# Kernel optimization log

Hardware: AMD Instinct MI355X
Metric: run time of the kernel (lower is better)

## Reference

```python
import jax, jax.numpy as jnp
import numpy as np

B = 4096          # graphs (frames)
NPG = 22          # players per frame
N = B * NPG       # total nodes
E = B * NPG * (NPG - 1)
D_BB = 256        # backbone_dout == GRNN hidden
D_NODE = 128      # raw node feature dim
D_PROJ = 256      # cfg.proj_dout
D_GIN = 64        # glob_din
D_GOUT = 128      # cfg.glob_dout
D_IN = D_BB + D_PROJ  # GRNN input dim = 512


def setup_inputs() -> dict:
    key = jax.random.key(0)
    ks = jax.random.split(key, 24)
    def w(k, shape):
        return jax.random.normal(k, shape, jnp.float32) * 0.05
    inp = {
        "z": jax.random.normal(ks[0], (N, D_BB), jnp.float32),
        "u": jax.random.normal(ks[1], (B, D_GIN), jnp.float32),
        "x": jax.random.normal(ks[2], (N, D_NODE), jnp.float32),
        # edge_index is unused math-wise because GConvGRU is built with K=1 ChebConvs
        "edge_index": jax.random.randint(ks[3], (2, E), 0, N, dtype=jnp.int32),
        "batch": jnp.repeat(jnp.arange(B, dtype=jnp.int32), NPG),
        "batch_size": B,
        "prev_h": jax.random.normal(ks[4], (N, D_BB), jnp.float32),
        # fusion params
        "w_proj": w(ks[5], (D_NODE, D_PROJ)), "b_proj": jnp.zeros((D_PROJ,), jnp.float32),
        "w_glob": w(ks[6], (D_GIN, D_GOUT)), "b_glob": jnp.zeros((D_GOUT,), jnp.float32),
        # GConvGRU (K=1 ChebConv == linear) gate params: update z, reset r, candidate h
        "W_xz": w(ks[7], (D_IN, D_BB)),  "b_xz": jnp.zeros((D_BB,), jnp.float32),
        "W_hz": w(ks[8], (D_BB, D_BB)),  "b_hz": jnp.zeros((D_BB,), jnp.float32),
        "W_xr": w(ks[9], (D_IN, D_BB)),  "b_xr": jnp.zeros((D_BB,), jnp.float32),
        "W_hr": w(ks[10], (D_BB, D_BB)), "b_hr": jnp.zeros((D_BB,), jnp.float32),
        "W_xh": w(ks[11], (D_IN, D_BB)), "b_xh": jnp.zeros((D_BB,), jnp.float32),
        "W_hh": w(ks[12], (D_BB, D_BB)), "b_hh": jnp.zeros((D_BB,), jnp.float32),
    }
    return inp


def reference(z, u, x, edge_index, batch, batch_size, prev_h,
              w_proj, b_proj, w_glob, b_glob,
              W_xz, b_xz, W_hz, b_hz,
              W_xr, b_xr, W_hr, b_hr,
              W_xh, b_xh, W_hh, b_hh):
    # --- GraphGlobalFusion: mean readout + relu(Linear(u)) + concat ---
    sums = jax.ops.segment_sum(z, batch, num_segments=batch_size)            # [B, D_BB]
    cnts = jax.ops.segment_sum(jnp.ones((z.shape[0], 1), z.dtype), batch,
                               num_segments=batch_size)                      # [B, 1]
    graph_emb = sums / jnp.maximum(cnts, 1.0)
    glob_emb = jax.nn.relu(u @ w_glob + b_glob)                              # [B, D_GOUT]
    fused = jnp.concatenate([graph_emb, glob_emb], axis=-1)                  # [B, D_BB+D_GOUT]

    # --- node mode: raw feature projection, then GConvGRU (K=1 -> linear gates) ---
    x_proj = jax.nn.relu(x @ w_proj + b_proj)                                # [N, D_PROJ]
    xin = jnp.concatenate([z, x_proj], axis=-1)                              # [N, D_IN]
    Z = jax.nn.sigmoid(xin @ W_xz + b_xz + prev_h @ W_hz + b_hz)
    R = jax.nn.sigmoid(xin @ W_xr + b_xr + prev_h @ W_hr + b_hr)
    H_tilde = jnp.tanh(xin @ W_xh + b_xh + (prev_h * R) @ W_hh + b_hh)
    h = Z * prev_h + (1.0 - Z) * H_tilde                                     # [N, D_BB]
    return (fused, h)
```

## Files before the change

### kernel.cpp

```cpp
#include <hip/hip_runtime.h>
#include <hip/hip_bf16.h>

#define NNODES 90112
#define BGRAPH 4096
#define NPG 22
#define DBB 256
#define DNODE 128
#define DPROJ 256
#define DGIN 64
#define DGOUT 128

#define WTG_OFF   32768
#define WTHH_OFF  622592
#define WS_BF16_ELEMS 688128

typedef __attribute__((ext_vector_type(8))) short bf16x8;
typedef __attribute__((ext_vector_type(4))) short bf16x4;
typedef __attribute__((ext_vector_type(4))) float f32x4;

__device__ __forceinline__ short f2bf(float f) {
  __hip_bfloat16 h = __float2bfloat16(f);
  return *reinterpret_cast<short*>(&h);
}
__device__ __forceinline__ float bf2f(short s) {
  union { unsigned int u; float f; } c;
  c.u = ((unsigned int)(unsigned short)s) << 16;
  return c.f;
}
__device__ __forceinline__ float fsig(float xv) {
  return __fdividef(1.0f, 1.0f + __expf(-xv));
}
__device__ __forceinline__ float ftanh(float xv) {
  return 1.0f - __fdividef(2.0f, __expf(2.0f * xv) + 1.0f);
}

#define DMA16(gsrc, ldst)                                                        \
  __builtin_amdgcn_global_load_lds(                                              \
      (const __attribute__((address_space(1))) void*)(gsrc),                     \
      (__attribute__((address_space(3))) void*)(ldst), 16, 0, 0)

#define VMWAIT(N) do { asm volatile("s_waitcnt vmcnt(" #N ")" ::: "memory");     \
                       __builtin_amdgcn_sched_barrier(0); } while (0)
#define LBAR() do { asm volatile("s_waitcnt lgkmcnt(0)" ::: "memory");           \
                    __builtin_amdgcn_s_barrier(); } while (0)

__global__ void pack_weights(const float* __restrict__ w_proj,
                             const float* __restrict__ W_xz, const float* __restrict__ W_hz,
                             const float* __restrict__ W_xr, const float* __restrict__ W_hr,
                             const float* __restrict__ W_xh, const float* __restrict__ W_hh,
                             const float* __restrict__ b_xz, const float* __restrict__ b_hz,
                             const float* __restrict__ b_xr, const float* __restrict__ b_hr,
                             const float* __restrict__ b_xh, const float* __restrict__ b_hh,
                             __hip_bfloat16* __restrict__ wsb, float* __restrict__ wsf) {
  int i = blockIdx.x * 256 + threadIdx.x;
  if (i < 32768) {
    int c = i >> 7, k = i & 127;
    wsb[i] = __float2bfloat16(w_proj[k * DPROJ + c]);
  } else if (i < WTHH_OFF) {
    int j = i - WTG_OFF;
    int kc  = j / 24576;
    int rem = j - kc * 24576;
    int ct  = rem >> 9;
    int q   = rem & 511;
    int l   = q >> 3, e = q & 7;
    int l15 = l & 15, kg = l >> 4;
    int k   = kc * 32 + kg * 8 + e;
    int g   = ct >> 4;
    int c   = (ct & 15) * 16 + l15;
    float v;
    if (g == 0)      v = (k < 512) ? W_xz[k * 256 + c] : W_hz[(k - 512) * 256 + c];
    else if (g == 1) v = (k < 512) ? W_xr[k * 256 + c] : W_hr[(k - 512) * 256 + c];
    else             v = (k < 512) ? W_xh[k * 256 + c] : 0.0f;
    wsb[i] = __float2bfloat16(v);
  } else if (i < WS_BF16_ELEMS) {
    int j = i - WTHH_OFF;
    int kc  = j >> 13;
    int rem = j & 8191;
    int ct  = rem >> 9;
    int q   = rem & 511;
    int l   = q >> 3, e = q & 7;
    int l15 = l & 15, kg = l >> 4;
    int k   = kc * 32 + kg * 8 + e;
    int c   = ct * 16 + l15;
    wsb[i] = __float2bfloat16(W_hh[k * 256 + c]);
  }
  if (i < 256) {
    wsf[i]       = b_xz[i] + b_hz[i];
    wsf[256 + i] = b_xr[i] + b_hr[i];
    wsf[512 + i] = b_xh[i] + b_hh[i];
  }
}

__global__ void fused_head(const float* __restrict__ z, const float* __restrict__ u,
                           const float* __restrict__ w_glob, const float* __restrict__ b_glob,
                           float* __restrict__ out) {
  int b = blockIdx.x;
  int t = threadIdx.x;
  __shared__ float us[DGIN];
  if (t < DGIN) us[t] = u[b * DGIN + t];
  __syncthreads();
  const float* zb = z + (size_t)b * NPG * DBB;
  #pragma unroll
  for (int half = 0; half < 2; ++half) {
    int c = t + half * 128;
    float s = 0.f;
    #pragma unroll
    for (int r = 0; r < NPG; ++r) s += zb[r * DBB + c];
    out[(size_t)b * 384 + c] = s * (1.0f / NPG);
  }
  float acc = b_glob[t];
  #pragma unroll
  for (int k = 0; k < DGIN; ++k) acc += us[k] * w_glob[k * DGOUT + t];
  out[(size_t)b * 384 + 256 + t] = fmaxf(acc, 0.f);
}

#define MFMA16(a, b, c) __builtin_amdgcn_mfma_f32_16x16x32_bf16(a, b, c, 0, 0, 0)

__global__ __launch_bounds__(1024)
void grnn_main(const float* __restrict__ z, const float* __restrict__ x,
               const float* __restrict__ prev_h, const float* __restrict__ b_proj,
               const __hip_bfloat16* __restrict__ wsb, const float* __restrict__ wsf,
               float* __restrict__ h_out) {
  __shared__ __align__(16) __hip_bfloat16 Wb[2][24576];
  __shared__ __align__(16) __hip_bfloat16 ActC[2][64 * 40];
  __shared__ __align__(16) __hip_bfloat16 XP[64 * 256];

  const int r0   = blockIdx.x * 64;
  const int tid  = threadIdx.x;
  const int wid  = tid >> 6;
  const int lane = tid & 63;
  const int l15  = lane & 15;
  const int lg   = lane >> 4;
  const int c0   = wid * 16;
  const int cgrp = (c0 >> 3) + (lg >> 1);
  const int lgl  = (lg & 1) * 4;

  const __hip_bfloat16* wpk = wsb + WTG_OFF;
  const __hip_bfloat16* hpk = wsb + WTHH_OFF;

  {
    int row = tid >> 4, c8 = tid & 15;
    const float* p = x + (size_t)(r0 + row) * DNODE + c8 * 8;
    f32x4 f0 = *(const f32x4*)p;
    f32x4 f1 = *(const f32x4*)(p + 4);
    bf16x8 o;
    o[0]=f2bf(f0[0]); o[1]=f2bf(f0[1]); o[2]=f2bf(f0[2]); o[3]=f2bf(f0[3]);
    o[4]=f2bf(f1[0]); o[5]=f2bf(f1[1]); o[6]=f2bf(f1[2]); o[7]=f2bf(f1[3]);
    *(bf16x8*)&Wb[1][row * 128 + (c8 ^ (row & 7)) * 8] = o;
  }
  __syncthreads();

  #pragma unroll
  for (int gs = 0; gs < 3; ++gs) {
    int ct = gs * 16 + wid;
    DMA16(wpk + ((size_t)(0 * 48 + ct) * 64 + lane) * 8, &Wb[0][ct * 512]);
  }
  f32x4 accp[4] = {};
  {
    const __hip_bfloat16* wp0 = wsb + (size_t)(c0 + l15) * DNODE + lg * 8;
    #pragma unroll
    for (int kb = 0; kb < 4; ++kb) {
      bf16x8 wp = *(const bf16x8*)(wp0 + kb * 32);
      const int gk = kb * 4 + lg;
      bf16x8 act[4];
      #pragma unroll
      for (int rt = 0; rt < 4; ++rt) {
        const int row = rt * 16 + l15;
        act[rt] = *(const bf16x8*)&Wb[1][row * 128 + (gk ^ (row & 7)) * 8];
      }
      __builtin_amdgcn_s_setprio(1);
      #pragma unroll
      for (int rt = 0; rt < 4; ++rt)
        accp[rt] = MFMA16(wp, act[rt], accp[rt]);
      __builtin_amdgcn_s_setprio(0);
    }
  }
  {
    float4 bp4 = *(const float4*)&b_proj[c0 + lg * 4];
    #pragma unroll
    for (int rt = 0; rt < 4; ++rt) {
      int r = rt * 16 + l15;
      bf16x4 o;
      o[0] = f2bf(fmaxf(accp[rt][0] + bp4.x, 0.f));
      o[1] = f2bf(fmaxf(accp[rt][1] + bp4.y, 0.f));
      o[2] = f2bf(fmaxf(accp[rt][2] + bp4.z, 0.f));
      o[3] = f2bf(fmaxf(accp[rt][3] + bp4.w, 0.f));
      *(bf16x4*)&XP[r * 256 + ((cgrp ^ (r & 7)) * 8) + lgl] = o;
    }
  }
  {
    int row = tid >> 4, c2 = (tid & 15) * 2;
    const float* p = z + (size_t)(r0 + row) * DBB + c2;
    float a = p[0], b = p[1];
    unsigned int pk = (unsigned int)(unsigned short)f2bf(a) |
                      ((unsigned int)(unsigned short)f2bf(b) << 16);
    *(unsigned int*)&ActC[0][row * 40 + (c2 >> 3) * 8 + (c2 & 7)] = pk;
  }
  __syncthreads();

  f32x4 accz[4] = {}, accr[4] = {}, acch[4] = {};
  #pragma unroll
  for (int kc = 0; kc < 24; ++kc) {
    const int kn = kc + 1;
    if (kn < 8 || (kn >= 16 && kn < 24)) {
      const float* src = (kn < 8) ? z : prev_h;
      const int kofs = (kn < 8 ? kn : kn - 16) * 32;
      int row = tid >> 4, c2 = (tid & 15) * 2;
      const float* p = src + (size_t)(r0 + row) * DBB + kofs + c2;
      float a = p[0], b = p[1];
      unsigned int pk = (unsigned int)(unsigned short)f2bf(a) |
                        ((unsigned int)(unsigned short)f2bf(b) << 16);
      *(unsigned int*)&ActC[kn & 1][row * 40 + (c2 >> 3) * 8 + (c2 & 7)] = pk;
    }
    __builtin_amdgcn_sched_barrier(0);
    if (kn < 24) {
      const int ns = (kn < 16) ? 3 : 2;
      #pragma unroll
      for (int gs = 0; gs < 3; ++gs) {
        if (gs < ns) {
          int ct = gs * 16 + wid;
          DMA16(wpk + ((size_t)(kn * 48 + ct) * 64 + lane) * 8, &Wb[kn & 1][ct * 512]);
        }
      }
    }
    __builtin_amdgcn_sched_barrier(0);
    if (kc < 8 || kc >= 16) LBAR();
    if (kc < 15)      VMWAIT(3);
    else if (kc < 23) VMWAIT(2);
    else              VMWAIT(0);
    bf16x8 act[4];
    #pragma unroll
    for (int rt = 0; rt < 4; ++rt) {
      const int row = rt * 16 + l15;
      if (kc < 8 || kc >= 16)
        act[rt] = *(const bf16x8*)&ActC[kc & 1][row * 40 + lg * 8];
      else {
        const int gk = (kc - 8) * 4 + lg;
        act[rt] = *(const bf16x8*)&XP[row * 256 + (gk ^ (row & 7)) * 8];
      }
    }
    bf16x8 wz = *(const bf16x8*)&Wb[kc & 1][(0 * 16 + wid) * 512 + lane * 8];
    bf16x8 wr = *(const bf16x8*)&Wb[kc & 1][(1 * 16 + wid) * 512 + lane * 8];
    bf16x8 wh;
    if (kc < 16) wh = *(const bf16x8*)&Wb[kc & 1][(2 * 16 + wid) * 512 + lane * 8];
    __builtin_amdgcn_s_setprio(1);
    #pragma unroll
    for (int rt = 0; rt < 4; ++rt) {
      accz[rt] = MFMA16(wz, act[rt], accz[rt]);
      accr[rt] = MFMA16(wr, act[rt], accr[rt]);
      if (kc < 16) acch[rt] = MFMA16(wh, act[rt], acch[rt]);
    }
    __builtin_amdgcn_s_setprio(0);
    if (kc < 7 || (kc >= 16 && kc < 23)) LBAR();
  }

  DMA16(hpk + ((size_t)(0 * 16 + wid) * 64 + lane) * 8, &Wb[0][wid * 512]);
  f32x4 phv[4];
  {
    float4 br4 = *(const float4*)&wsf[256 + c0 + lg * 4];
    #pragma unroll
    for (int rt = 0; rt < 4; ++rt) {
      int r = rt * 16 + l15;
      phv[rt] = *(const f32x4*)&prev_h[(size_t)(r0 + r) * DBB + c0 + lg * 4];
      bf16x4 o;
      o[0] = f2bf(phv[rt][0] * fsig(accr[rt][0] + br4.x));
      o[1] = f2bf(phv[rt][1] * fsig(accr[rt][1] + br4.y));
      o[2] = f2bf(phv[rt][2] * fsig(accr[rt][2] + br4.z));
      o[3] = f2bf(phv[rt][3] * fsig(accr[rt][3] + br4.w));
      *(bf16x4*)&XP[r * 256 + ((cgrp ^ (r & 7)) * 8) + lgl] = o;
    }
  }
  LBAR();

  #pragma unroll
  for (int s = 0; s < 8; ++s) {
    if (s < 7)
      DMA16(hpk + ((size_t)((s + 1) * 16 + wid) * 64 + lane) * 8, &Wb[(s + 1) & 1][wid * 512]);
    __builtin_amdgcn_sched_barrier(0);
    if (s < 7) VMWAIT(1); else VMWAIT(0);
    bf16x8 act[4];
    #pragma unroll
    for (int rt = 0; rt < 4; ++rt) {
      const int row = rt * 16 + l15;
      const int gk = s * 4 + lg;
      act[rt] = *(const bf16x8*)&XP[row * 256 + (gk ^ (row & 7)) * 8];
    }
    bf16x8 wv = *(const bf16x8*)&Wb[s & 1][wid * 512 + lane * 8];
    __builtin_amdgcn_s_setprio(1);
    #pragma unroll
    for (int rt = 0; rt < 4; ++rt)
      acch[rt] = MFMA16(wv, act[rt], acch[rt]);
    __builtin_amdgcn_s_setprio(0);
  }

  {
    float4 bz4 = *(const float4*)&wsf[c0 + lg * 4];
    float4 bh4 = *(const float4*)&wsf[512 + c0 + lg * 4];
    #pragma unroll
    for (int rt = 0; rt < 4; ++rt) {
      int r = rt * 16 + l15;
      f32x4 hv;
      float zg = fsig(accz[rt][0] + bz4.x);
      hv[0] = zg * phv[rt][0] + (1.f - zg) * ftanh(acch[rt][0] + bh4.x);
      zg = fsig(accz[rt][1] + bz4.y);
      hv[1] = zg * phv[rt][1] + (1.f - zg) * ftanh(acch[rt][1] + bh4.y);
      zg = fsig(accz[rt][2] + bz4.z);
      hv[2] = zg * phv[rt][2] + (1.f - zg) * ftanh(acch[rt][2] + bh4.z);
      zg = fsig(accz[rt][3] + bz4.w);
      hv[3] = zg * phv[rt][3] + (1.f - zg) * ftanh(acch[rt][3] + bh4.w);
      *(f32x4*)&h_out[(size_t)(r0 + r) * DBB + c0 + lg * 4] = hv;
    }
  }
}

extern "C" void kernel_launch(void* const* d_in, const int* in_sizes, int n_in,
                              void* d_out, int out_size, void* d_ws, size_t ws_size,
                              hipStream_t stream) {
  const float* z      = (const float*)d_in[0];
  const float* u      = (const float*)d_in[1];
  const float* x      = (const float*)d_in[2];
  const float* prev_h = (const float*)d_in[6];
  const float* w_proj = (const float*)d_in[7];
  const float* b_proj = (const float*)d_in[8];
  const float* w_glob = (const float*)d_in[9];
  const float* b_glob = (const float*)d_in[10];
  const float* W_xz   = (const float*)d_in[11];
  const float* b_xz   = (const float*)d_in[12];
  const float* W_hz   = (const float*)d_in[13];
  const float* b_hz   = (const float*)d_in[14];
  const float* W_xr   = (const float*)d_in[15];
  const float* b_xr   = (const float*)d_in[16];
  const float* W_hr   = (const float*)d_in[17];
  const float* b_hr   = (const float*)d_in[18];
  const float* W_xh   = (const float*)d_in[19];
  const float* b_xh   = (const float*)d_in[20];
  const float* W_hh   = (const float*)d_in[21];
  const float* b_hh   = (const float*)d_in[22];

  __hip_bfloat16* wsb = (__hip_bfloat16*)d_ws;
  float* wsf = (float*)((char*)d_ws + (size_t)WS_BF16_ELEMS * 2);

  float* fused = (float*)d_out;
  float* h_out = fused + (size_t)BGRAPH * 384;

  pack_weights<<<dim3(WS_BF16_ELEMS / 256), dim3(256), 0, stream>>>(
      w_proj, W_xz, W_hz, W_xr, W_hr, W_xh, W_hh,
      b_xz, b_hz, b_xr, b_hr, b_xh, b_hh, wsb, wsf);

  fused_head<<<dim3(BGRAPH), dim3(128), 0, stream>>>(z, u, w_glob, b_glob, fused);

  grnn_main<<<dim3(NNODES / 64), dim3(1024), 0, stream>>>(
      z, x, prev_h, b_proj, wsb, wsf, h_out);
}
```

Baseline: 234.8 us.

## Deepen weight DMA pipeline to two stages ahead with per-gate waits

```diff
diff --git a/kernel.cpp b/kernel.cpp
--- a/kernel.cpp
+++ b/kernel.cpp
@@ -17,6 +17,7 @@
 typedef __attribute__((ext_vector_type(8))) short bf16x8;
 typedef __attribute__((ext_vector_type(4))) short bf16x4;
 typedef __attribute__((ext_vector_type(4))) float f32x4;
+typedef __attribute__((ext_vector_type(2))) float f32x2;
 
 __device__ __forceinline__ short f2bf(float f) {
   __hip_bfloat16 h = __float2bfloat16(f);
@@ -39,8 +40,18 @@
       (const __attribute__((address_space(1))) void*)(gsrc),                     \
       (__attribute__((address_space(3))) void*)(ldst), 16, 0, 0)
 
-#define VMWAIT(N) do { asm volatile("s_waitcnt vmcnt(" #N ")" ::: "memory");     \
-                       __builtin_amdgcn_sched_barrier(0); } while (0)
+template<int N>
+__device__ __forceinline__ void vmwaitN() {
+  static_assert(N >= 0 && N <= 6, "vmcnt range");
+  if constexpr (N == 0) asm volatile("s_waitcnt vmcnt(0)" ::: "memory");
+  else if constexpr (N == 1) asm volatile("s_waitcnt vmcnt(1)" ::: "memory");
+  else if constexpr (N == 2) asm volatile("s_waitcnt vmcnt(2)" ::: "memory");
+  else if constexpr (N == 3) asm volatile("s_waitcnt vmcnt(3)" ::: "memory");
+  else if constexpr (N == 4) asm volatile("s_waitcnt vmcnt(4)" ::: "memory");
+  else if constexpr (N == 5) asm volatile("s_waitcnt vmcnt(5)" ::: "memory");
+  else asm volatile("s_waitcnt vmcnt(6)" ::: "memory");
+  __builtin_amdgcn_sched_barrier(0);
+}
 #define LBAR() do { asm volatile("s_waitcnt lgkmcnt(0)" ::: "memory");           \
                     __builtin_amdgcn_s_barrier(); } while (0)
 
@@ -116,14 +127,118 @@
 
 #define MFMA16(a, b, c) __builtin_amdgcn_mfma_f32_16x16x32_bf16(a, b, c, 0, 0, 0)
 
+template<int KC>
+__device__ __forceinline__ void gstep(
+    const float* __restrict__ z, const float* __restrict__ prev_h,
+    const __hip_bfloat16* __restrict__ wpk,
+    __hip_bfloat16* Wb, __hip_bfloat16* ActC, __hip_bfloat16* XP,
+    int tid, int r0, int l15, int lg, int wid, int lane,
+    f32x4 (&accz)[4], f32x4 (&accr)[4], f32x4 (&acch)[4]) {
+  constexpr int  KN       = KC + 1;
+  constexpr bool do_stage = (KN >= 1 && KN <= 7) || (KN >= 16 && KN <= 23);
+  constexpr bool bar      = (KC >= 1 && KC <= 7) || (KC >= 15 && KC <= 23);
+  constexpr bool staged   = (KC < 8) || (KC >= 16);
+  constexpr bool has_h    = (KC < 16);
+  constexpr int NZ = (KC <= 14) ? 5 : (KC == 15) ? 4 : (KC <= 22) ? 3 : 1;
+  constexpr int NR = (KC <= 14) ? 5 : (KC == 15) ? 4 : (KC <= 21) ? 3 : (KC == 22) ? 2 : 0;
+  constexpr int NH = (KC <= 14) ? 5 : 4;
+
+  f32x2 sl;
+  int srow = tid >> 4, sc2 = (tid & 15) * 2;
+  if constexpr (do_stage) {
+    const float* src = (KN < 8) ? z : prev_h;
+    constexpr int kofs = (KN < 8 ? KN : KN - 16) * 32;
+    sl = *(const f32x2*)(src + (size_t)(r0 + srow) * DBB + kofs + sc2);
+  }
+  if constexpr (bar) LBAR();
+
+  bf16x8 act[4];
+  #pragma unroll
+  for (int rt = 0; rt < 4; ++rt) {
+    const int row = rt * 16 + l15;
+    if constexpr (staged)
+      act[rt] = *(const bf16x8*)&ActC[(KC % 3) * (64 * 40) + row * 40 + lg * 8];
+    else {
+      const int gk = (KC - 8) * 4 + lg;
+      act[rt] = *(const bf16x8*)&XP[row * 256 + ((gk ^ (row & 7)) * 8)];
+    }
+  }
+
+  vmwaitN<NZ>();
+  {
+    bf16x8 w = *(const bf16x8*)&Wb[((KC & 1) * 3 + 0) * 8192 + wid * 512 + lane * 8];
+    __builtin_amdgcn_s_setprio(1);
+    #pragma unroll
+    for (int rt = 0; rt < 4; ++rt) accz[rt] = MFMA16(w, act[rt], accz[rt]);
+    __builtin_amdgcn_s_setprio(0);
+  }
+  if constexpr (KC + 2 <= 23)
+    DMA16(wpk + (((size_t)(KC + 2) * 48 + 0 * 16 + wid) * 64 + lane) * 8,
+          Wb + (((KC + 2) & 1) * 3 + 0) * 8192 + wid * 512);
+
+  vmwaitN<NR>();
+  {
+    bf16x8 w = *(const bf16x8*)&Wb[((KC & 1) * 3 + 1) * 8192 + wid * 512 + lane * 8];
+    __builtin_amdgcn_s_setprio(1);
+    #pragma unroll
+    for (int rt = 0; rt < 4; ++rt) accr[rt] = MFMA16(w, act[rt], accr[rt]);
+    __builtin_amdgcn_s_setprio(0);
+  }
+  if constexpr (KC + 2 <= 23)
+    DMA16(wpk + (((size_t)(KC + 2) * 48 + 1 * 16 + wid) * 64 + lane) * 8,
+          Wb + (((KC + 2) & 1) * 3 + 1) * 8192 + wid * 512);
+
+  if constexpr (has_h) {
+    vmwaitN<NH>();
+    bf16x8 w = *(const bf16x8*)&Wb[((KC & 1) * 3 + 2) * 8192 + wid * 512 + lane * 8];
+    __builtin_amdgcn_s_setprio(1);
+    #pragma unroll
+    for (int rt = 0; rt < 4; ++rt) acch[rt] = MFMA16(w, act[rt], acch[rt]);
+    __builtin_amdgcn_s_setprio(0);
+    if constexpr (KC + 2 <= 15)
+      DMA16(wpk + (((size_t)(KC + 2) * 48 + 2 * 16 + wid) * 64 + lane) * 8,
+            Wb + (((KC + 2) & 1) * 3 + 2) * 8192 + wid * 512);
+  }
+
+  if constexpr (do_stage) {
+    unsigned int pk = (unsigned int)(unsigned short)f2bf(sl[0]) |
+                      ((unsigned int)(unsigned short)f2bf(sl[1]) << 16);
+    *(unsigned int*)&ActC[(KN % 3) * (64 * 40) + srow * 40 + sc2] = pk;
+  }
+}
+
+template<int S>
+__device__ __forceinline__ void hstep(
+    const __hip_bfloat16* __restrict__ hpk, __hip_bfloat16* Wb, __hip_bfloat16* XP,
+    int l15, int lg, int wid, int lane, f32x4 (&acch)[4]) {
+  constexpr int NW = (S <= 5) ? 2 : (S == 6) ? 1 : 0;
+  bf16x8 act[4];
+  #pragma unroll
+  for (int rt = 0; rt < 4; ++rt) {
+    const int row = rt * 16 + l15;
+    const int gk = S * 4 + lg;
+    act[rt] = *(const bf16x8*)&XP[row * 256 + ((gk ^ (row & 7)) * 8)];
+  }
+  vmwaitN<NW>();
+  bf16x8 w = *(const bf16x8*)&Wb[(S % 4) * 8192 + wid * 512 + lane * 8];
+  __builtin_amdgcn_s_setprio(1);
+  #pragma unroll
+  for (int rt = 0; rt < 4; ++rt) acch[rt] = MFMA16(w, act[rt], acch[rt]);
+  __builtin_amdgcn_s_setprio(0);
+  if constexpr (S + 3 <= 7)
+    DMA16(hpk + (((size_t)(S + 3) * 16 + wid) * 64 + lane) * 8,
+          Wb + ((S + 3) % 4) * 8192 + wid * 512);
+}
+
 __global__ __launch_bounds__(1024)
 void grnn_main(const float* __restrict__ z, const float* __restrict__ x,
                const float* __restrict__ prev_h, const float* __restrict__ b_proj,
                const __hip_bfloat16* __restrict__ wsb, const float* __restrict__ wsf,
                float* __restrict__ h_out) {
-  __shared__ __align__(16) __hip_bfloat16 Wb[2][24576];
-  __shared__ __align__(16) __hip_bfloat16 ActC[2][64 * 40];
+  __shared__ __align__(16) __hip_bfloat16 Wb[6 * 8192];
+  __shared__ __align__(16) __hip_bfloat16 Xs[64 * 128];
   __shared__ __align__(16) __hip_bfloat16 XP[64 * 256];
+  __shared__ __align__(16) __hip_bfloat16 ActC[3 * 64 * 40];
 
   const int r0   = blockIdx.x * 64;
   const int tid  = threadIdx.x;
@@ -146,14 +261,14 @@
     bf16x8 o;
     o[0]=f2bf(f0[0]); o[1]=f2bf(f0[1]); o[2]=f2bf(f0[2]); o[3]=f2bf(f0[3]);
     o[4]=f2bf(f1[0]); o[5]=f2bf(f1[1]); o[6]=f2bf(f1[2]); o[7]=f2bf(f1[3]);
-    *(bf16x8*)&Wb[1][row * 128 + (c8 ^ (row & 7)) * 8] = o;
+    *(bf16x8*)&Xs[row * 128 + (c8 ^ (row & 7)) * 8] = o;
   }
   __syncthreads();
 
-  #pragma unroll
-  for (int gs = 0; gs < 3; ++gs) {
-    int ct = gs * 16 + wid;
-    DMA16(wpk + ((size_t)(0 * 48 + ct) * 64 + lane) * 8, &Wb[0][ct * 512]);
+  f32x2 sl0;
+  {
+    int row = tid >> 4, c2 = (tid & 15) * 2;
+    sl0 = *(const f32x2*)(z + (size_t)(r0 + row) * DBB + c2);
   }
   f32x4 accp[4] = {};
   {
@@ -166,7 +281,7 @@
       #pragma unroll
       for (int rt = 0; rt < 4; ++rt) {
         const int row = rt * 16 + l15;
-        act[rt] = *(const bf16x8*)&Wb[1][row * 128 + (gk ^ (row & 7)) * 8];
+        act[rt] = *(const bf16x8*)&Xs[row * 128 + (gk ^ (row & 7)) * 8];
       }
       __builtin_amdgcn_s_setprio(1);
       #pragma unroll
@@ -174,6 +289,18 @@
         accp[rt] = MFMA16(wp, act[rt], accp[rt]);
       __builtin_amdgcn_s_setprio(0);
     }
+  }
+  #pragma unroll
+  for (int c = 0; c < 2; ++c)
+    #pragma unroll
+    for (int g = 0; g < 3; ++g)
+      DMA16(wpk + (((size_t)c * 48 + g * 16 + wid) * 64 + lane) * 8,
+            Wb + ((c & 1) * 3 + g) * 8192 + wid * 512);
+  {
+    int row = tid >> 4, c2 = (tid & 15) * 2;
+    unsigned int pk = (unsigned int)(unsigned short)f2bf(sl0[0]) |
+                      ((unsigned int)(unsigned short)f2bf(sl0[1]) << 16);
+    *(unsigned int*)&ActC[0 * (64 * 40) + row * 40 + c2] = pk;
   }
   {
     float4 bp4 = *(const float4*)&b_proj[c0 + lg * 4];
@@ -188,73 +315,18 @@
       *(bf16x4*)&XP[r * 256 + ((cgrp ^ (r & 7)) * 8) + lgl] = o;
     }
   }
-  {
-    int row = tid >> 4, c2 = (tid & 15) * 2;
-    const float* p = z + (size_t)(r0 + row) * DBB + c2;
-    float a = p[0], b = p[1];
-    unsigned int pk = (unsigned int)(unsigned short)f2bf(a) |
-                      ((unsigned int)(unsigned short)f2bf(b) << 16);
-    *(unsigned int*)&ActC[0][row * 40 + (c2 >> 3) * 8 + (c2 & 7)] = pk;
-  }
-  __syncthreads();
+  LBAR();
 
   f32x4 accz[4] = {}, accr[4] = {}, acch[4] = {};
-  #pragma unroll
-  for (int kc = 0; kc < 24; ++kc) {
-    const int kn = kc + 1;
-    if (kn < 8 || (kn >= 16 && kn < 24)) {
-      const float* src = (kn < 8) ? z : prev_h;
-      const int kofs = (kn < 8 ? kn : kn - 16) * 32;
-      int row = tid >> 4, c2 = (tid & 15) * 2;
-      const float* p = src + (size_t)(r0 + row) * DBB + kofs + c2;
-      float a = p[0], b = p[1];
-      unsigned int pk = (unsigned int)(unsigned short)f2bf(a) |
-                        ((unsigned int)(unsigned short)f2bf(b) << 16);
-      *(unsigned int*)&ActC[kn & 1][row * 40 + (c2 >> 3) * 8 + (c2 & 7)] = pk;
-    }
-    __builtin_amdgcn_sched_barrier(0);
-    if (kn < 24) {
-      const int ns = (kn < 16) ? 3 : 2;
-      #pragma unroll
-      for (int gs = 0; gs < 3; ++gs) {
-        if (gs < ns) {
-          int ct = gs * 16 + wid;
-          DMA16(wpk + ((size_t)(kn * 48 + ct) * 64 + lane) * 8, &Wb[kn & 1][ct * 512]);
-        }
-      }
-    }
-    __builtin_amdgcn_sched_barrier(0);
-    if (kc < 8 || kc >= 16) LBAR();
-    if (kc < 15)      VMWAIT(3);
-    else if (kc < 23) VMWAIT(2);
-    else              VMWAIT(0);
-    bf16x8 act[4];
-    #pragma unroll
-    for (int rt = 0; rt < 4; ++rt) {
-      const int row = rt * 16 + l15;
-      if (kc < 8 || kc >= 16)
-        act[rt] = *(const bf16x8*)&ActC[kc & 1][row * 40 + lg * 8];
-      else {
-        const int gk = (kc - 8) * 4 + lg;
-        act[rt] = *(const bf16x8*)&XP[row * 256 + (gk ^ (row & 7)) * 8];
-      }
-    }
-    bf16x8 wz = *(const bf16x8*)&Wb[kc & 1][(0 * 16 + wid) * 512 + lane * 8];
-    bf16x8 wr = *(const bf16x8*)&Wb[kc & 1][(1 * 16 + wid) * 512 + lane * 8];
-    bf16x8 wh;
-    if (kc < 16) wh = *(const bf16x8*)&Wb[kc & 1][(2 * 16 + wid) * 512 + lane * 8];
-    __builtin_amdgcn_s_setprio(1);
-    #pragma unroll
-    for (int rt = 0; rt < 4; ++rt) {
-      accz[rt] = MFMA16(wz, act[rt], accz[rt]);
-      accr[rt] = MFMA16(wr, act[rt], accr[rt]);
-      if (kc < 16) acch[rt] = MFMA16(wh, act[rt], acch[rt]);
-    }
-    __builtin_amdgcn_s_setprio(0);
-    if (kc < 7 || (kc >= 16 && kc < 23)) LBAR();
-  }
-
-  DMA16(hpk + ((size_t)(0 * 16 + wid) * 64 + lane) * 8, &Wb[0][wid * 512]);
+  #define GS(K) gstep<K>(z, prev_h, wpk, Wb, ActC, XP, tid, r0, l15, lg, wid, lane, accz, accr, acch)
+  GS(0);  GS(1);  GS(2);  GS(3);  GS(4);  GS(5);  GS(6);  GS(7);
+  GS(8);  GS(9);  GS(10); GS(11); GS(12); GS(13); GS(14); GS(15);
+  GS(16); GS(17); GS(18); GS(19); GS(20); GS(21); GS(22); GS(23);
+  #undef GS
+
+  #pragma unroll
+  for (int s = 0; s < 3; ++s)
+    DMA16(hpk + (((size_t)s * 16 + wid) * 64 + lane) * 8, Wb + (s % 4) * 8192 + wid * 512);
   f32x4 phv[4];
   {
     float4 br4 = *(const float4*)&wsf[256 + c0 + lg * 4];
@@ -272,26 +344,9 @@
   }
   LBAR();
 
-  #pragma unroll
-  for (int s = 0; s < 8; ++s) {
-    if (s < 7)
-      DMA16(hpk + ((size_t)((s + 1) * 16 + wid) * 64 + lane) * 8, &Wb[(s + 1) & 1][wid * 512]);
-    __builtin_amdgcn_sched_barrier(0);
-    if (s < 7) VMWAIT(1); else VMWAIT(0);
-    bf16x8 act[4];
-    #pragma unroll
-    for (int rt = 0; rt < 4; ++rt) {
-      const int row = rt * 16 + l15;
-      const int gk = s * 4 + lg;
-      act[rt] = *(const bf16x8*)&XP[row * 256 + (gk ^ (row & 7)) * 8];
-    }
-    bf16x8 wv = *(const bf16x8*)&Wb[s & 1][wid * 512 + lane * 8];
-    __builtin_amdgcn_s_setprio(1);
-    #pragma unroll
-    for (int rt = 0; rt < 4; ++rt)
-      acch[rt] = MFMA16(wv, act[rt], acch[rt]);
-    __builtin_amdgcn_s_setprio(0);
-  }
+  #define HS(S) hstep<S>(hpk, Wb, XP, l15, lg, wid, lane, acch)
+  HS(0); HS(1); HS(2); HS(3); HS(4); HS(5); HS(6); HS(7);
+  #undef HS
 
   {
     float4 bz4 = *(const float4*)&wsf[c0 + lg * 4];
```

New measurement: 211.4 us. 1.11x faster.
